# Optimization experiments

Hardware: AMD Instinct MI355X
Metric: run time of the kernel (lower is better)

## Reference

```python
import jax, jax.numpy as jnp
import numpy as np

B, N = 16, 4096
COORD, VAL = 2, 3
LD = 256          # latent_dim / code_dim
NC = 1024         # num_codes
HID = 256         # hidden_size
NL = 5            # num_layers
NV = 4            # num_latent_vectors (residual VQ stages)
NI = 1000         # num_images
CC = 0.25         # commitment_cost
OMEGA = 30.0


def setup_inputs() -> dict:
    key = jax.random.key(0)
    ks = jax.random.split(key, 12)
    coords = jax.random.uniform(ks[0], (B, N, COORD), jnp.float32, -1.0, 1.0)
    latent_indices = jax.random.randint(ks[1], (B,), 0, NI)
    latents = jax.random.normal(ks[2], (NI, NV, LD), jnp.float32)
    emb = jax.random.normal(ks[3], (NV, NC, LD), jnp.float32)
    emb = emb / jnp.linalg.norm(emb, axis=-1, keepdims=True)
    mod_W = jax.random.normal(ks[4], (NL, LD, 2 * HID), jnp.float32) * (1.0 / np.sqrt(LD))
    mod_b = jnp.zeros((NL, 2 * HID), jnp.float32)
    # SIREN init
    W0 = jax.random.uniform(ks[5], (COORD, HID), jnp.float32, -1.0 / COORD, 1.0 / COORD)
    b0 = jax.random.uniform(ks[6], (HID,), jnp.float32, -1.0 / np.sqrt(COORD), 1.0 / np.sqrt(COORD))
    w_bound = np.sqrt(6.0 / HID) / OMEGA
    Wh = jax.random.uniform(ks[7], (NL - 1, HID, HID), jnp.float32, -w_bound, w_bound)
    bh = jax.random.uniform(ks[8], (NL - 1, HID), jnp.float32, -1.0 / np.sqrt(HID), 1.0 / np.sqrt(HID))
    Wl = jax.random.uniform(ks[9], (HID, VAL), jnp.float32, -w_bound, w_bound)
    bl = jax.random.uniform(ks[10], (VAL,), jnp.float32, -1.0 / np.sqrt(HID), 1.0 / np.sqrt(HID))
    return {"coords": coords, "latent_indices": latent_indices, "latents": latents,
            "emb": emb, "mod_W": mod_W, "mod_b": mod_b, "W0": W0, "b0": b0,
            "Wh": Wh, "bh": bh, "Wl": Wl, "bl": bl}


def reference(coords, latent_indices, latents, emb, mod_W, mod_b, W0, b0, Wh, bh, Wl, bl):
    sg = jax.lax.stop_gradient
    # per-image latent, summed over latent vectors -> [B, LD]
    img_latents = latents[latent_indices]
    z = img_latents.sum(axis=1)
    residual = z
    z_q_sum = jnp.zeros_like(z)
    vq_loss = jnp.float32(0.0)
    for s in range(NV):  # fixed small residual-VQ stage loop
        E = emb[s]  # [NC, LD]
        # squared euclidean distances [B, NC]
        dist = (jnp.sum(residual ** 2, axis=1, keepdims=True)
                - 2.0 * residual @ E.T + jnp.sum(E ** 2, axis=1))
        idx = jnp.argmin(dist, axis=1)
        z_q = E[idx]  # [B, LD]
        z_q_st = residual + sg(z_q - residual)  # straight-through
        vq_loss = vq_loss + CC * jnp.mean((sg(z_q) - residual) ** 2)
        z_q_sum = z_q_sum + z_q_st
        residual = sg(residual - z_q_st)
    vq_loss = vq_loss / NV
    effective_z = z_q_sum  # eval: no warmup scaling
    # FiLM params per layer: [B, NL, 2*HID]
    mods = jnp.einsum('bd,ldh->blh', effective_z, mod_W) + mod_b
    gam, bet = jnp.split(mods, 2, axis=-1)  # each [B, NL, HID]
    # SIREN decoder, keeping [B, N, HID] layout
    x = jnp.sin(OMEGA * (coords @ W0 + b0))
    for i in range(1, NL):
        pre = x @ Wh[i - 1] + bh[i - 1]
        pre = pre * (1.0 + gam[:, i, None, :]) + bet[:, i, None, :]
        x = jnp.sin(OMEGA * pre)
    values = x @ Wl + bl  # [B, N, VAL]
    return values, vq_loss
```

## Files before the change

kernel.cpp:

```cpp
#include <hip/hip_runtime.h>
#include <math.h>

#define LDIM 256
#define NCODES 1024
#define HID 256
#define NLAY 5
#define NVQ 4
#define CC_ 0.25f
#define OMEGA_ 30.0f
#define BATCH 16
#define NPTS 4096
#define PTILE 128


typedef __attribute__((ext_vector_type(8))) short short8;
typedef __attribute__((ext_vector_type(4))) float f32x4;

__device__ __forceinline__ unsigned int pack_split(float x) {
  unsigned int u = __builtin_bit_cast(unsigned int, x);
  float hf = __builtin_bit_cast(float, u & 0xffff0000u);
  float lf = x - hf;
  unsigned int ul = __builtin_bit_cast(unsigned int, lf);
  return (u & 0xffff0000u) | (ul >> 16);
}
__device__ __forceinline__ void split_trunc(float x, short& hi, short& lo) {
  unsigned int u = __builtin_bit_cast(unsigned int, x);
  float hf = __builtin_bit_cast(float, u & 0xffff0000u);
  float lf = x - hf;
  hi = (short)(u >> 16);
  lo = (short)(__builtin_bit_cast(unsigned int, lf) >> 16);
}
__device__ __forceinline__ float bf16_hi_f(unsigned short h) {
  return __builtin_bit_cast(float, (unsigned int)h << 16);
}

__global__ __launch_bounds__(256) void vq_init(const int* __restrict__ lidx,
                                               const float* __restrict__ latents,
                                               float* __restrict__ ws) {
  const int t = threadIdx.x, b = blockIdx.x;
  const int ib = lidx[b];
  float z = 0.f;
  #pragma unroll
  for (int v = 0; v < NVQ; ++v) z += latents[((size_t)ib * NVQ + v) * LDIM + t];
  ws[b * LDIM + t] = z;
  ws[4096 + b * LDIM + t] = 0.f;
  if (t == 0) ws[8192 + b] = 0.f;
}

__global__ __launch_bounds__(256) void vq_scan(const float* __restrict__ emb,
                                               float* __restrict__ ws, int stage) {
  __shared__ __align__(16) float Ech[32 * 260];
  __shared__ __align__(16) float r_s[LDIM];
  __shared__ float mval[256];
  __shared__ int   midx[256];
  const int t = threadIdx.x;
  const int b = blockIdx.x >> 3;
  const int slice = blockIdx.x & 7;
  r_s[t] = ws[b * LDIM + t];
  __syncthreads();
  const float* E = emb + (size_t)stage * NCODES * LDIM + (size_t)slice * 128 * LDIM;
  const float4* E4 = (const float4*)E;
  const int cg = t >> 3;
  const int dq = t & 7;
  float bestv = 3.4e38f; int besti = 0;
  for (int ch = 0; ch < 4; ++ch) {
    __syncthreads();
    #pragma unroll
    for (int it = 0; it < 8; ++it) {
      int f = it * 256 + t;
      int row = f >> 6;
      int col4 = f & 63;
      *(float4*)&Ech[row * 260 + col4 * 4] = E4[(size_t)(ch * 32 + row) * 64 + col4];
    }
    __syncthreads();
    float dot = 0.f, e2 = 0.f;
    const float* er = &Ech[cg * 260];
    const float4* rr4 = (const float4*)r_s;
    #pragma unroll
    for (int j = 0; j < 8; ++j) {
      int d4 = dq + 8 * j;
      float4 e = *(const float4*)&er[d4 * 4];
      float4 r = rr4[d4];
      dot += e.x * r.x + e.y * r.y + e.z * r.z + e.w * r.w;
      e2  += e.x * e.x + e.y * e.y + e.z * e.z + e.w * e.w;
    }
    dot += __shfl_xor(dot, 1); e2 += __shfl_xor(e2, 1);
    dot += __shfl_xor(dot, 2); e2 += __shfl_xor(e2, 2);
    dot += __shfl_xor(dot, 4); e2 += __shfl_xor(e2, 4);
    if (dq == 0) {
      float dist = e2 - 2.f * dot;
      int c = slice * 128 + ch * 32 + cg;
      if (dist < bestv) { bestv = dist; besti = c; }
    }
  }
  mval[t] = (dq == 0) ? bestv : 3.4e38f;
  midx[t] = (dq == 0) ? besti : (1 << 30);
  __syncthreads();
  for (int off = 128; off > 0; off >>= 1) {
    if (t < off) {
      float ov = mval[t + off]; int oi = midx[t + off];
      if (ov < mval[t] || (ov == mval[t] && oi < midx[t])) { mval[t] = ov; midx[t] = oi; }
    }
    __syncthreads();
  }
  if (t == 0) {
    ws[8208 + b * 8 + slice] = mval[0];
    ((int*)ws)[8336 + b * 8 + slice] = midx[0];
  }
}

__global__ __launch_bounds__(256) void vq_update(const float* __restrict__ emb,
                                                 float* __restrict__ ws, int stage) {
  __shared__ int bestIdx;
  __shared__ float red[256];
  const int t = threadIdx.x;
  const int b = blockIdx.x;
  if (t == 0) {
    float bv = ws[8208 + b * 8];
    int bi = ((const int*)ws)[8336 + b * 8];
    for (int s2 = 1; s2 < 8; ++s2) {
      float v = ws[8208 + b * 8 + s2];
      int i2 = ((const int*)ws)[8336 + b * 8 + s2];
      if (v < bv || (v == bv && i2 < bi)) { bv = v; bi = i2; }
    }
    bestIdx = bi;
  }
  __syncthreads();
  const float* E = emb + (size_t)stage * NCODES * LDIM;
  float r = ws[b * LDIM + t];
  float zq = E[(size_t)bestIdx * LDIM + t];
  float diff = zq - r;
  red[t] = diff * diff;
  __syncthreads();
  for (int off = 128; off > 0; off >>= 1) {
    if (t < off) red[t] += red[t + off];
    __syncthreads();
  }
  if (t == 0) ws[8192 + b] += red[0];
  ws[4096 + b * LDIM + t] += zq;
  ws[b * LDIM + t] = r - zq;
}

__global__ __launch_bounds__(256) void film_kernel(const float* __restrict__ mod_W,
                                                   const float* __restrict__ mod_b,
                                                   float* __restrict__ ws,
                                                   float* __restrict__ loss_out) {
  __shared__ float z_s[LDIM];
  const int t = threadIdx.x;
  if (blockIdx.x == 0 && t == 0) {
    float s = 0.f;
    for (int i = 0; i < BATCH; ++i) s += ws[8192 + i];
    loss_out[0] = s * (CC_ / (NVQ * BATCH * LDIM));
  }
  __syncthreads();
  const int li = blockIdx.x & 3;
  const int b  = blockIdx.x >> 2;
  const int l  = li + 1;
  z_s[t] = ws[4096 + b * LDIM + t];
  __syncthreads();
  float m1 = mod_b[l * 2 * HID + t];
  float m2 = mod_b[l * 2 * HID + HID + t];
  const float* Wm = mod_W + (size_t)l * LDIM * 2 * HID;
  #pragma unroll 4
  for (int d = 0; d < LDIM; ++d) {
    float zd = z_s[d];
    m1 = fmaf(zd, Wm[d * 2 * HID + t], m1);
    m2 = fmaf(zd, Wm[d * 2 * HID + HID + t], m2);
  }
  float* film = ws + 8192;
  film[((b * 4 + li) * 2 + 0) * HID + t] = 1.f + m1;
  film[((b * 4 + li) * 2 + 1) * HID + t] = m2;
}

__global__ __launch_bounds__(512) void siren_mfma(
    const float* __restrict__ coords,
    const float* __restrict__ W0,
    const float* __restrict__ b0,
    const float* __restrict__ Whg,
    const float* __restrict__ bhv,
    const float* __restrict__ Wl,
    const float* __restrict__ bl,
    const float* __restrict__ ws,
    float* __restrict__ out) {
  __shared__ unsigned int x_u[128 * 260];
  __shared__ float osum[128 * 4 * 3];
  const int tid = threadIdx.x;
  const int bp = blockIdx.x;
  const int b = bp >> 5;
  const int tile = bp & 31;
  const int pbase = b * NPTS + tile * PTILE;

  {
    const int quarter = tid >> 7;
    const int p = tid & 127;
    const float c0 = coords[(size_t)(pbase + p) * 2 + 0];
    const float c1 = coords[(size_t)(pbase + p) * 2 + 1];
    const int d0 = quarter * 64;
    for (int i = 0; i < 64; i += 4) {
      unsigned int buf[4];
      #pragma unroll
      for (int j = 0; j < 4; ++j) {
        int d = d0 + i + j;
        float pre = fmaf(c0, W0[d], fmaf(c1, W0[HID + d], b0[d]));
        buf[j] = pack_split(__sinf(OMEGA_ * pre));
      }
      *(uint4*)&x_u[p * 260 + d0 + i] = *(uint4*)buf;
    }
  }

  const int lane = tid & 63;
  const int wv = tid >> 6;
  const int pg = wv & 1;
  const int hq = wv >> 1;
  const int pb = pg * 64;
  const int hb = hq * 64;
  const int n = lane & 15;
  const int q = lane >> 4;

  const float* film = ws + 8192;

  for (int layer = 1; layer < NLAY; ++layer) {
    const int li = layer - 1;
    f32x4 acc[4][4];
    #pragma unroll
    for (int pt = 0; pt < 4; ++pt)
      #pragma unroll
      for (int ht = 0; ht < 4; ++ht)
        acc[pt][ht] = (f32x4){0.f, 0.f, 0.f, 0.f};

    __syncthreads();

    for (int kc = 0; kc < HID; kc += 32) {
      short8 Bh[4], Bl[4];
      #pragma unroll
      for (int ht = 0; ht < 4; ++ht) {
        const float* wbase = Whg + ((size_t)(li * 256 + kc + q * 8)) * 256 + hb + ht * 16 + n;
        #pragma unroll
        for (int j = 0; j < 8; ++j) {
          short hi, lo;
          split_trunc(wbase[(size_t)j * 256], hi, lo);
          Bh[ht][j] = hi; Bl[ht][j] = lo;
        }
      }
      short8 ah[4], al[4];
      #pragma unroll
      for (int pt = 0; pt < 4; ++pt) {
        const uint4* ap = (const uint4*)&x_u[(pb + pt * 16 + n) * 260 + kc + q * 8];
        uint4 a0 = ap[0], a1 = ap[1];
        unsigned int aw[8] = {a0.x, a0.y, a0.z, a0.w, a1.x, a1.y, a1.z, a1.w};
        #pragma unroll
        for (int j = 0; j < 8; ++j) {
          ah[pt][j] = (short)(aw[j] >> 16);
          al[pt][j] = (short)(aw[j] & 0xffffu);
        }
      }
      #pragma unroll
      for (int ht = 0; ht < 4; ++ht) {
        #pragma unroll
        for (int pt = 0; pt < 4; ++pt) {
          acc[pt][ht] = __builtin_amdgcn_mfma_f32_16x16x32_bf16(ah[pt], Bh[ht], acc[pt][ht], 0, 0, 0);
          acc[pt][ht] = __builtin_amdgcn_mfma_f32_16x16x32_bf16(ah[pt], Bl[ht], acc[pt][ht], 0, 0, 0);
          acc[pt][ht] = __builtin_amdgcn_mfma_f32_16x16x32_bf16(al[pt], Bh[ht], acc[pt][ht], 0, 0, 0);
        }
      }
    }

    __syncthreads();

    #pragma unroll
    for (int ht = 0; ht < 4; ++ht) {
      const int h = hb + ht * 16 + n;
      const float bias = bhv[li * HID + h];
      const float g1 = film[((b * 4 + li) * 2 + 0) * HID + h];
      const float bt = film[((b * 4 + li) * 2 + 1) * HID + h];
      #pragma unroll
      for (int pt = 0; pt < 4; ++pt) {
        #pragma unroll
        for (int r = 0; r < 4; ++r) {
          float pre = acc[pt][ht][r] + bias;
          pre = fmaf(pre, g1, bt);
          x_u[(pb + pt * 16 + q * 4 + r) * 260 + h] = pack_split(__sinf(OMEGA_ * pre));
        }
      }
    }
  }
  __syncthreads();

  {
    const int p = tid >> 2;
    const int dq = tid & 3;
    float v0 = 0.f, v1 = 0.f, v2 = 0.f;
    for (int i = 0; i < 64; ++i) {
      int d = dq * 64 + i;
      unsigned int wrd = x_u[p * 260 + d];
      float xv = bf16_hi_f((unsigned short)(wrd >> 16)) +
                 bf16_hi_f((unsigned short)(wrd & 0xffffu));
      v0 = fmaf(xv, Wl[d * 3 + 0], v0);
      v1 = fmaf(xv, Wl[d * 3 + 1], v1);
      v2 = fmaf(xv, Wl[d * 3 + 2], v2);
    }
    osum[(p * 4 + dq) * 3 + 0] = v0;
    osum[(p * 4 + dq) * 3 + 1] = v1;
    osum[(p * 4 + dq) * 3 + 2] = v2;
  }
  __syncthreads();
  if (tid < PTILE) {
    const int p = tid;
    float v[3] = {bl[0], bl[1], bl[2]};
    #pragma unroll
    for (int dq = 0; dq < 4; ++dq)
      #pragma unroll
      for (int c = 0; c < 3; ++c) v[c] += osum[(p * 4 + dq) * 3 + c];
    size_t o = (size_t)(pbase + p) * 3;
    out[o + 0] = v[0]; out[o + 1] = v[1]; out[o + 2] = v[2];
  }
}

extern "C" void kernel_launch(void* const* d_in, const int* in_sizes, int n_in,
                              void* d_out, int out_size, void* d_ws, size_t ws_size,
                              hipStream_t stream) {
  (void)in_sizes; (void)n_in; (void)ws_size;
  const float* coords  = (const float*)d_in[0];
  const int*   lidx    = (const int*)d_in[1];
  const float* latents = (const float*)d_in[2];
  const float* emb     = (const float*)d_in[3];
  const float* mod_W   = (const float*)d_in[4];
  const float* mod_b   = (const float*)d_in[5];
  const float* W0      = (const float*)d_in[6];
  const float* b0      = (const float*)d_in[7];
  const float* Wh      = (const float*)d_in[8];
  const float* bh      = (const float*)d_in[9];
  const float* Wl      = (const float*)d_in[10];
  const float* bl      = (const float*)d_in[11];
  float* out = (float*)d_out;
  float* ws  = (float*)d_ws;
  float* loss_out = out + (out_size - 1);

  vq_init<<<BATCH, 256, 0, stream>>>(lidx, latents, ws);
  for (int s = 0; s < NVQ; ++s) {
    vq_scan<<<BATCH * 8, 256, 0, stream>>>(emb, ws, s);
    vq_update<<<BATCH, 256, 0, stream>>>(emb, ws, s);
  }
  film_kernel<<<BATCH * 4, 256, 0, stream>>>(mod_W, mod_b, ws, loss_out);
  siren_mfma<<<(BATCH * NPTS) / PTILE, 512, 0, stream>>>(coords, W0, b0, Wh, bh, Wl, bl, ws, out);
}
```

Baseline: 272.5 us.

## Pre-split hidden weights to bf16 hi/lo and merge VQ stages via atomicMin

A new prep kernel transposes each hidden weight matrix once and splits it into bf16 hi/lo arrays in workspace. The SIREN kernel then loads ready-made B fragments instead of converting fp32 weights inside the inner loop, and keeps activations as separate hi/lo short arrays in LDS. The VQ path replaces the scan+update kernel pair per stage with a single kernel that picks the winning code through a packed 64-bit atomicMin, and rebuilds the residual, loss and quantized sum from the stored indices. This removes launches and per-layer conversion work, at the cost of needing a large workspace (with a fallback to the old kernel) and an extra prep launch on every call.

```diff
diff --git a/kernel.cpp b/kernel.cpp
--- a/kernel.cpp
+++ b/kernel.cpp
@@ -12,6 +12,10 @@
 #define NPTS 4096
 #define PTILE 128
 
+#define WIN_OFF 4096
+#define FILM_OFF 8192
+#define WP_BYTE 196608
+#define FAST_WS_NEEDED 1245184u
 
 typedef __attribute__((ext_vector_type(8))) short short8;
 typedef __attribute__((ext_vector_type(4))) float f32x4;
@@ -32,6 +36,10 @@
 }
 __device__ __forceinline__ float bf16_hi_f(unsigned short h) {
   return __builtin_bit_cast(float, (unsigned int)h << 16);
+}
+__device__ __forceinline__ unsigned int mono_u32(float f) {
+  unsigned int u = __builtin_bit_cast(unsigned int, f);
+  return (u & 0x80000000u) ? ~u : (u | 0x80000000u);
 }
 
 __global__ __launch_bounds__(256) void vq_init(const int* __restrict__ lidx,
@@ -43,12 +51,11 @@
   #pragma unroll
   for (int v = 0; v < NVQ; ++v) z += latents[((size_t)ib * NVQ + v) * LDIM + t];
   ws[b * LDIM + t] = z;
-  ws[4096 + b * LDIM + t] = 0.f;
-  if (t == 0) ws[8192 + b] = 0.f;
-}
-
-__global__ __launch_bounds__(256) void vq_scan(const float* __restrict__ emb,
-                                               float* __restrict__ ws, int stage) {
+  if (t < NVQ) ((unsigned long long*)(ws + WIN_OFF))[b * NVQ + t] = ~0ULL;
+}
+
+__global__ __launch_bounds__(256) void vq_stage(const float* __restrict__ emb,
+                                                float* __restrict__ ws, int stage) {
   __shared__ __align__(16) float Ech[32 * 260];
   __shared__ __align__(16) float r_s[LDIM];
   __shared__ float mval[256];
@@ -56,7 +63,13 @@
   const int t = threadIdx.x;
   const int b = blockIdx.x >> 3;
   const int slice = blockIdx.x & 7;
-  r_s[t] = ws[b * LDIM + t];
+  const unsigned long long* wsl = (const unsigned long long*)(ws + WIN_OFF);
+  float r = ws[b * LDIM + t];
+  for (int j = 0; j < stage; ++j) {
+    int wj = (int)(wsl[b * NVQ + j] & 0xffffffffULL);
+    r -= emb[((size_t)j * NCODES + wj) * LDIM + t];
+  }
+  r_s[t] = r;
   __syncthreads();
   const float* E = emb + (size_t)stage * NCODES * LDIM + (size_t)slice * 128 * LDIM;
   const float4* E4 = (const float4*)E;
@@ -80,8 +93,8 @@
     for (int j = 0; j < 8; ++j) {
       int d4 = dq + 8 * j;
       float4 e = *(const float4*)&er[d4 * 4];
-      float4 r = rr4[d4];
-      dot += e.x * r.x + e.y * r.y + e.z * r.z + e.w * r.w;
+      float4 rv = rr4[d4];
+      dot += e.x * rv.x + e.y * rv.y + e.z * rv.z + e.w * rv.w;
       e2  += e.x * e.x + e.y * e.y + e.z * e.z + e.w * e.w;
     }
     dot += __shfl_xor(dot, 1); e2 += __shfl_xor(e2, 1);
@@ -104,59 +117,56 @@
     __syncthreads();
   }
   if (t == 0) {
-    ws[8208 + b * 8 + slice] = mval[0];
-    ((int*)ws)[8336 + b * 8 + slice] = midx[0];
-  }
-}
-
-__global__ __launch_bounds__(256) void vq_update(const float* __restrict__ emb,
-                                                 float* __restrict__ ws, int stage) {
-  __shared__ int bestIdx;
+    unsigned long long pack =
+        ((unsigned long long)mono_u32(mval[0]) << 32) | (unsigned int)midx[0];
+    atomicMin((unsigned long long*)(ws + WIN_OFF) + (b * NVQ + stage), pack);
+  }
+}
+
+__global__ __launch_bounds__(256) void vq_loss(const float* __restrict__ emb,
+                                               const float* __restrict__ ws,
+                                               float* __restrict__ loss_out) {
   __shared__ float red[256];
   const int t = threadIdx.x;
-  const int b = blockIdx.x;
-  if (t == 0) {
-    float bv = ws[8208 + b * 8];
-    int bi = ((const int*)ws)[8336 + b * 8];
-    for (int s2 = 1; s2 < 8; ++s2) {
-      float v = ws[8208 + b * 8 + s2];
-      int i2 = ((const int*)ws)[8336 + b * 8 + s2];
-      if (v < bv || (v == bv && i2 < bi)) { bv = v; bi = i2; }
-    }
-    bestIdx = bi;
-  }
-  __syncthreads();
-  const float* E = emb + (size_t)stage * NCODES * LDIM;
-  float r = ws[b * LDIM + t];
-  float zq = E[(size_t)bestIdx * LDIM + t];
-  float diff = zq - r;
-  red[t] = diff * diff;
+  const unsigned long long* wsl = (const unsigned long long*)(ws + WIN_OFF);
+  float acc = 0.f;
+  for (int b = 0; b < BATCH; ++b) {
+    float r = ws[b * LDIM + t];
+    #pragma unroll
+    for (int s = 0; s < NVQ; ++s) {
+      int w = (int)(wsl[b * NVQ + s] & 0xffffffffULL);
+      float e = emb[((size_t)s * NCODES + w) * LDIM + t];
+      float d = e - r;
+      acc += d * d;
+      r -= e;
+    }
+  }
+  red[t] = acc;
   __syncthreads();
   for (int off = 128; off > 0; off >>= 1) {
     if (t < off) red[t] += red[t + off];
     __syncthreads();
   }
-  if (t == 0) ws[8192 + b] += red[0];
-  ws[4096 + b * LDIM + t] += zq;
-  ws[b * LDIM + t] = r - zq;
-}
-
-__global__ __launch_bounds__(256) void film_kernel(const float* __restrict__ mod_W,
+  if (t == 0) loss_out[0] = red[0] * (CC_ / (NVQ * BATCH * LDIM));
+}
+
+__global__ __launch_bounds__(256) void film_kernel(const float* __restrict__ emb,
+                                                   const float* __restrict__ mod_W,
                                                    const float* __restrict__ mod_b,
-                                                   float* __restrict__ ws,
-                                                   float* __restrict__ loss_out) {
+                                                   float* __restrict__ ws) {
   __shared__ float z_s[LDIM];
   const int t = threadIdx.x;
-  if (blockIdx.x == 0 && t == 0) {
-    float s = 0.f;
-    for (int i = 0; i < BATCH; ++i) s += ws[8192 + i];
-    loss_out[0] = s * (CC_ / (NVQ * BATCH * LDIM));
-  }
-  __syncthreads();
   const int li = blockIdx.x & 3;
   const int b  = blockIdx.x >> 2;
   const int l  = li + 1;
-  z_s[t] = ws[4096 + b * LDIM + t];
+  const unsigned long long* wsl = (const unsigned long long*)(ws + WIN_OFF);
+  float z = 0.f;
+  #pragma unroll
+  for (int s = 0; s < NVQ; ++s) {
+    int w = (int)(wsl[b * NVQ + s] & 0xffffffffULL);
+    z += emb[((size_t)s * NCODES + w) * LDIM + t];
+  }
+  z_s[t] = z;
   __syncthreads();
   float m1 = mod_b[l * 2 * HID + t];
   float m2 = mod_b[l * 2 * HID + HID + t];
@@ -167,9 +177,178 @@
     m1 = fmaf(zd, Wm[d * 2 * HID + t], m1);
     m2 = fmaf(zd, Wm[d * 2 * HID + HID + t], m2);
   }
-  float* film = ws + 8192;
+  float* film = ws + FILM_OFF;
   film[((b * 4 + li) * 2 + 0) * HID + t] = 1.f + m1;
   film[((b * 4 + li) * 2 + 1) * HID + t] = m2;
+}
+
+__global__ __launch_bounds__(256) void prep_w(const float* __restrict__ Whg,
+                                              float* __restrict__ ws) {
+  __shared__ float st[64][257];
+  const int t = threadIdx.x;
+  const int li = blockIdx.x & 3;
+  const int kc0 = (blockIdx.x >> 2) * 64;
+  for (int r = 0; r < 64; ++r)
+    st[r][t] = Whg[((size_t)(li * 256 + kc0 + r)) * 256 + t];
+  __syncthreads();
+  short* wp_hi = (short*)((char*)ws + WP_BYTE);
+  short* wp_lo = wp_hi + 4 * 256 * 256;
+  const size_t base = ((size_t)(li * 256 + t)) * 256 + kc0;
+  for (int i0 = 0; i0 < 64; i0 += 8) {
+    short8 hv, lv;
+    #pragma unroll
+    for (int j = 0; j < 8; ++j) {
+      short hi, lo;
+      split_trunc(st[i0 + j][t], hi, lo);
+      hv[j] = hi; lv[j] = lo;
+    }
+    *(short8*)&wp_hi[base + i0] = hv;
+    *(short8*)&wp_lo[base + i0] = lv;
+  }
+}
+
+__global__ __launch_bounds__(512) void siren_mfma_fast(
+    const float* __restrict__ coords,
+    const float* __restrict__ W0,
+    const float* __restrict__ b0,
+    const float* __restrict__ bhv,
+    const float* __restrict__ Wl,
+    const float* __restrict__ bl,
+    const float* __restrict__ ws,
+    float* __restrict__ out) {
+  __shared__ short x_h[128 * 264];
+  __shared__ short x_l[128 * 264];
+  __shared__ float osum[128 * 4 * 3];
+  const int tid = threadIdx.x;
+  const int bp = blockIdx.x;
+  const int b = bp >> 5;
+  const int tile = bp & 31;
+  const int pbase = b * NPTS + tile * PTILE;
+
+  {
+    const int quarter = tid >> 7;
+    const int p = tid & 127;
+    const float c0 = coords[(size_t)(pbase + p) * 2 + 0];
+    const float c1 = coords[(size_t)(pbase + p) * 2 + 1];
+    const int d0 = quarter * 64;
+    for (int i = 0; i < 64; i += 8) {
+      short8 hv, lv;
+      #pragma unroll
+      for (int j = 0; j < 8; ++j) {
+        int d = d0 + i + j;
+        float pre = fmaf(c0, W0[d], fmaf(c1, W0[HID + d], b0[d]));
+        short hi, lo;
+        split_trunc(__sinf(OMEGA_ * pre), hi, lo);
+        hv[j] = hi; lv[j] = lo;
+      }
+      *(short8*)&x_h[p * 264 + d0 + i] = hv;
+      *(short8*)&x_l[p * 264 + d0 + i] = lv;
+    }
+  }
+
+  const int lane = tid & 63;
+  const int wv = tid >> 6;
+  const int pg = wv & 1;
+  const int hq = wv >> 1;
+  const int pb = pg * 64;
+  const int hb = hq * 64;
+  const int n = lane & 15;
+  const int q = lane >> 4;
+
+  const short* wp_hi = (const short*)((const char*)ws + WP_BYTE);
+  const short* wp_lo = wp_hi + 4 * 256 * 256;
+  const float* film = ws + FILM_OFF;
+
+  for (int layer = 1; layer < NLAY; ++layer) {
+    const int li = layer - 1;
+    f32x4 acc[4][4];
+    #pragma unroll
+    for (int pt = 0; pt < 4; ++pt)
+      #pragma unroll
+      for (int ht = 0; ht < 4; ++ht)
+        acc[pt][ht] = (f32x4){0.f, 0.f, 0.f, 0.f};
+
+    __syncthreads();
+
+    #pragma unroll 2
+    for (int kc = 0; kc < HID; kc += 32) {
+      short8 Bh[4], Bl[4];
+      #pragma unroll
+      for (int ht = 0; ht < 4; ++ht) {
+        const size_t wb = ((size_t)(li * 256 + hb + ht * 16 + n)) * 256 + kc + q * 8;
+        Bh[ht] = *(const short8*)&wp_hi[wb];
+        Bl[ht] = *(const short8*)&wp_lo[wb];
+      }
+      short8 Ah[4], Al[4];
+      #pragma unroll
+      for (int pt = 0; pt < 4; ++pt) {
+        const int xb = (pb + pt * 16 + n) * 264 + kc + q * 8;
+        Ah[pt] = *(const short8*)&x_h[xb];
+        Al[pt] = *(const short8*)&x_l[xb];
+      }
+      #pragma unroll
+      for (int ht = 0; ht < 4; ++ht) {
+        #pragma unroll
+        for (int pt = 0; pt < 4; ++pt) {
+          acc[pt][ht] = __builtin_amdgcn_mfma_f32_16x16x32_bf16(Ah[pt], Bh[ht], acc[pt][ht], 0, 0, 0);
+          acc[pt][ht] = __builtin_amdgcn_mfma_f32_16x16x32_bf16(Ah[pt], Bl[ht], acc[pt][ht], 0, 0, 0);
+          acc[pt][ht] = __builtin_amdgcn_mfma_f32_16x16x32_bf16(Al[pt], Bh[ht], acc[pt][ht], 0, 0, 0);
+        }
+      }
+    }
+
+    __syncthreads();
+
+    #pragma unroll
+    for (int ht = 0; ht < 4; ++ht) {
+      const int h = hb + ht * 16 + n;
+      const float bias = bhv[li * HID + h];
+      const float g1 = film[((b * 4 + li) * 2 + 0) * HID + h];
+      const float bt = film[((b * 4 + li) * 2 + 1) * HID + h];
+      #pragma unroll
+      for (int pt = 0; pt < 4; ++pt) {
+        #pragma unroll
+        for (int r = 0; r < 4; ++r) {
+          float pre = acc[pt][ht][r] + bias;
+          pre = fmaf(pre, g1, bt);
+          short hi, lo;
+          split_trunc(__sinf(OMEGA_ * pre), hi, lo);
+          const int row = pb + pt * 16 + q * 4 + r;
+          x_h[row * 264 + h] = hi;
+          x_l[row * 264 + h] = lo;
+        }
+      }
+    }
+  }
+  __syncthreads();
+
+  {
+    const int p = tid >> 2;
+    const int dq = tid & 3;
+    float v0 = 0.f, v1 = 0.f, v2 = 0.f;
+    for (int i = 0; i < 64; ++i) {
+      int d = dq * 64 + i;
+      float xv = bf16_hi_f((unsigned short)x_h[p * 264 + d]) +
+                 bf16_hi_f((unsigned short)x_l[p * 264 + d]);
+      v0 = fmaf(xv, Wl[d * 3 + 0], v0);
+      v1 = fmaf(xv, Wl[d * 3 + 1], v1);
+      v2 = fmaf(xv, Wl[d * 3 + 2], v2);
+    }
+    osum[(p * 4 + dq) * 3 + 0] = v0;
+    osum[(p * 4 + dq) * 3 + 1] = v1;
+    osum[(p * 4 + dq) * 3 + 2] = v2;
+  }
+  __syncthreads();
+  if (tid < PTILE) {
+    const int p = tid;
+    float v[3] = {bl[0], bl[1], bl[2]};
+    #pragma unroll
+    for (int dq = 0; dq < 4; ++dq)
+      #pragma unroll
+      for (int c = 0; c < 3; ++c) v[c] += osum[(p * 4 + dq) * 3 + c];
+    size_t o = (size_t)(pbase + p) * 3;
+    out[o + 0] = v[0]; out[o + 1] = v[1]; out[o + 2] = v[2];
+  }
 }
 
 __global__ __launch_bounds__(512) void siren_mfma(
@@ -189,7 +368,6 @@
   const int b = bp >> 5;
   const int tile = bp & 31;
   const int pbase = b * NPTS + tile * PTILE;
-
   {
     const int quarter = tid >> 7;
     const int p = tid & 127;
@@ -207,7 +385,6 @@
       *(uint4*)&x_u[p * 260 + d0 + i] = *(uint4*)buf;
     }
   }
-
   const int lane = tid & 63;
   const int wv = tid >> 6;
   const int pg = wv & 1;
@@ -216,9 +393,7 @@
   const int hb = hq * 64;
   const int n = lane & 15;
   const int q = lane >> 4;
-
-  const float* film = ws + 8192;
-
+  const float* film = ws + FILM_OFF;
   for (int layer = 1; layer < NLAY; ++layer) {
     const int li = layer - 1;
     f32x4 acc[4][4];
@@ -227,9 +402,7 @@
       #pragma unroll
       for (int ht = 0; ht < 4; ++ht)
         acc[pt][ht] = (f32x4){0.f, 0.f, 0.f, 0.f};
-
-    __syncthreads();
-
+    __syncthreads();
     for (int kc = 0; kc < HID; kc += 32) {
       short8 Bh[4], Bl[4];
       #pragma unroll
@@ -264,9 +437,7 @@
         }
       }
     }
-
-    __syncthreads();
-
+    __syncthreads();
     #pragma unroll
     for (int ht = 0; ht < 4; ++ht) {
       const int h = hb + ht * 16 + n;
@@ -285,7 +456,6 @@
     }
   }
   __syncthreads();
-
   {
     const int p = tid >> 2;
     const int dq = tid & 3;
@@ -319,7 +489,7 @@
 extern "C" void kernel_launch(void* const* d_in, const int* in_sizes, int n_in,
                               void* d_out, int out_size, void* d_ws, size_t ws_size,
                               hipStream_t stream) {
-  (void)in_sizes; (void)n_in; (void)ws_size;
+  (void)in_sizes; (void)n_in;
   const float* coords  = (const float*)d_in[0];
   const int*   lidx    = (const int*)d_in[1];
   const float* latents = (const float*)d_in[2];
@@ -336,11 +506,15 @@
   float* ws  = (float*)d_ws;
   float* loss_out = out + (out_size - 1);
 
+  const bool fast = (ws_size >= FAST_WS_NEEDED);
+  if (fast) prep_w<<<16, 256, 0, stream>>>(Wh, ws);
   vq_init<<<BATCH, 256, 0, stream>>>(lidx, latents, ws);
-  for (int s = 0; s < NVQ; ++s) {
-    vq_scan<<<BATCH * 8, 256, 0, stream>>>(emb, ws, s);
-    vq_update<<<BATCH, 256, 0, stream>>>(emb, ws, s);
-  }
-  film_kernel<<<BATCH * 4, 256, 0, stream>>>(mod_W, mod_b, ws, loss_out);
-  siren_mfma<<<(BATCH * NPTS) / PTILE, 512, 0, stream>>>(coords, W0, b0, Wh, bh, Wl, bl, ws, out);
-}
+  for (int s = 0; s < NVQ; ++s)
+    vq_stage<<<BATCH * 8, 256, 0, stream>>>(emb, ws, s);
+  vq_loss<<<1, 256, 0, stream>>>(emb, ws, loss_out);
+  film_kernel<<<BATCH * 4, 256, 0, stream>>>(emb, mod_W, mod_b, ws);
+  if (fast)
+    siren_mfma_fast<<<(BATCH * NPTS) / PTILE, 512, 0, stream>>>(coords, W0, b0, bh, Wl, bl, ws, out);
+  else
+    siren_mfma<<<(BATCH * NPTS) / PTILE, 512, 0, stream>>>(coords, W0, b0, Wh, bh, Wl, bl, ws, out);
+}
```

After: 320.9 us. +17.7%, slower.
